# Optimization experiments

Hardware: AMD Instinct MI355X
Metric: run time of the kernel (lower is better)

Reference implementation:

```python
import jax, jax.numpy as jnp
import numpy as np

N = 100000      # nodes
E = 1600000     # edges (avg degree 16)
DIN = 3         # input_dim (xyz coords)
DOUT = 64       # output_dim
EPS = 1e-5      # LayerNorm eps


def setup_inputs() -> dict:
    key = jax.random.key(0)
    ks = jax.random.split(key, 6)
    x = jax.random.normal(ks[0], (N, DIN), jnp.float32)
    edge_index = jax.random.randint(ks[1], (2, E), 0, N, dtype=jnp.int64)
    # li1: Linear(DIN, DOUT)
    W1 = jax.random.normal(ks[2], (DIN, DOUT), jnp.float32) / np.sqrt(DIN)
    b1 = jnp.zeros((DOUT,), jnp.float32)
    # gcn1: GCNConv(DOUT, DOUT) -> weight + bias
    Wg = jax.random.normal(ks[3], (DOUT, DOUT), jnp.float32) / np.sqrt(DOUT)
    bg = jnp.zeros((DOUT,), jnp.float32)
    # norm1d: LayerNorm(2*DOUT)
    gamma = jnp.ones((2 * DOUT,), jnp.float32)
    beta = jnp.zeros((2 * DOUT,), jnp.float32)
    return {"x": x, "edge_index": edge_index, "W1": W1, "b1": b1,
            "Wg": Wg, "bg": bg, "gamma": gamma, "beta": beta}


def reference(x, edge_index, W1, b1, Wg, bg, gamma, beta):
    n = x.shape[0]
    # li1 + act
    h = jax.nn.relu(x @ W1 + b1)                       # [N, DOUT]
    # GCNConv: add self loops, symmetric normalization D^-1/2 (A+I) D^-1/2
    loops = jnp.arange(n, dtype=edge_index.dtype)
    src = jnp.concatenate([edge_index[0], loops])      # [E+N]
    dst = jnp.concatenate([edge_index[1], loops])      # [E+N]
    deg = jax.ops.segment_sum(jnp.ones_like(dst, h.dtype), dst, num_segments=n)
    dinv = jnp.where(deg > 0, jax.lax.rsqrt(jnp.maximum(deg, 1.0)), 0.0)
    norm = dinv[src] * dinv[dst]                       # [E+N]
    hg = h @ Wg                                        # [N, DOUT]
    agg = jax.ops.segment_sum(hg[src] * norm[:, None], dst, num_segments=n)
    h2 = jax.nn.relu(agg + bg)                         # [N, DOUT]
    # concat + LayerNorm(2*DOUT)
    cat = jnp.concatenate([h, h2], axis=1)             # [N, 2*DOUT]
    mu = jnp.mean(cat, axis=-1, keepdims=True)
    var = jnp.mean(jnp.square(cat - mu), axis=-1, keepdims=True)
    return (cat - mu) * jax.lax.rsqrt(var + EPS) * gamma + beta
```

## Files before the change

kernel.cpp:

```cpp
#include <hip/hip_runtime.h>
#include <math.h>

#define N_NODES 100000
#define N_EDGES 1600000
#define EPS_    1e-5f
#define PAD     64
#define SCOL    48


#define NCHUNK_E 782
#define EPB_E    2048
#define NB_EDGE  (NCHUNK_E * 8)
#define PART_SZ  12500

#define LIN_WAVES 1563

typedef float v16f __attribute__((ext_vector_type(16)));

__device__ __forceinline__ float bf2f(unsigned short u) {
    union { unsigned int i; float f; } v; v.i = (unsigned int)u << 16; return v.f;
}
__device__ __forceinline__ unsigned short f2bf(float f) {
    union { float f; unsigned int i; } v; v.f = f;
    unsigned int b = v.i + 0x7FFFu + ((v.i >> 16) & 1u);
    return (unsigned short)(b >> 16);
}
__device__ __forceinline__ unsigned int pk2(float lo, float hi) {
    return (unsigned int)f2bf(lo) | ((unsigned int)f2bf(hi) << 16);
}

#define FMA16(A, wv0, wv1, wv2, wv3)                                          \
    do {                                                                      \
        A[0]  = fmaf(hk, wv0.x, A[0]);  A[1]  = fmaf(hk, wv0.y, A[1]);        \
        A[2]  = fmaf(hk, wv0.z, A[2]);  A[3]  = fmaf(hk, wv0.w, A[3]);        \
        A[4]  = fmaf(hk, wv1.x, A[4]);  A[5]  = fmaf(hk, wv1.y, A[5]);        \
        A[6]  = fmaf(hk, wv1.z, A[6]);  A[7]  = fmaf(hk, wv1.w, A[7]);        \
        A[8]  = fmaf(hk, wv2.x, A[8]);  A[9]  = fmaf(hk, wv2.y, A[9]);        \
        A[10] = fmaf(hk, wv2.z, A[10]); A[11] = fmaf(hk, wv2.w, A[11]);       \
        A[12] = fmaf(hk, wv3.x, A[12]); A[13] = fmaf(hk, wv3.y, A[13]);       \
        A[14] = fmaf(hk, wv3.z, A[14]); A[15] = fmaf(hk, wv3.w, A[15]);       \
    } while (0)

__global__ void fused_edge_lin_kernel(const int* __restrict__ src,
                                      const int* __restrict__ dst,
                                      const float* __restrict__ x,
                                      const float* __restrict__ W1,
                                      const float* __restrict__ b1,
                                      const float* __restrict__ Wg,
                                      int* __restrict__ cnt,
                                      int* __restrict__ ell,
                                      unsigned short* __restrict__ hb_g)
{
    const int tl    = threadIdx.x;
    const int part  = blockIdx.x & 7;
    const int chunk = blockIdx.x >> 3;
    const int lo    = part * PART_SZ;
    const int hi    = lo + PART_SZ;

    const int ebase = chunk * EPB_E + tl * 8;
    int dv[8], sv[8], pos[8];
    if (ebase + 8 <= N_EDGES) {
        const int4 d0 = *(const int4*)(dst + ebase);
        const int4 d1 = *(const int4*)(dst + ebase + 4);
        const int4 s0 = *(const int4*)(src + ebase);
        const int4 s1 = *(const int4*)(src + ebase + 4);
        dv[0] = d0.x; dv[1] = d0.y; dv[2] = d0.z; dv[3] = d0.w;
        dv[4] = d1.x; dv[5] = d1.y; dv[6] = d1.z; dv[7] = d1.w;
        sv[0] = s0.x; sv[1] = s0.y; sv[2] = s0.z; sv[3] = s0.w;
        sv[4] = s1.x; sv[5] = s1.y; sv[6] = s1.z; sv[7] = s1.w;
    } else {
#pragma unroll
        for (int j = 0; j < 8; ++j) {
            const int e = ebase + j;
            if (e < N_EDGES) { dv[j] = dst[e]; sv[j] = src[e]; }
            else             { dv[j] = -1;     sv[j] = 0;      }
        }
    }
#pragma unroll
    for (int j = 0; j < 8; ++j) {
        pos[j] = -1;
        if (dv[j] >= lo && dv[j] < hi) pos[j] = atomicAdd(&cnt[dv[j]], 1);
    }

    const int wave = blockIdx.x * 4 + (tl >> 6);
    if (wave < LIN_WAVES) {
        const int lane = tl & 63;
        const int n    = wave * 64 + lane;
        const bool act = (n < N_NODES);
        float x0 = 0.f, x1 = 0.f, x2 = 0.f;
        if (act) { x0 = x[n * 3]; x1 = x[n * 3 + 1]; x2 = x[n * 3 + 2]; }

        v16f a0, a1, a2, a3;
#pragma unroll
        for (int i = 0; i < 16; ++i) { a0[i] = 0.f; a1[i] = 0.f; a2[i] = 0.f; a3[i] = 0.f; }

        for (int k = 0; k < 64; ++k) {
            const float w0 = W1[k];
            const float w1 = W1[64 + k];
            const float w2 = W1[128 + k];
            const float bb = b1[k];
            const float hk = fmaxf(fmaf(x0, w0, fmaf(x1, w1, fmaf(x2, w2, bb))), 0.f);

            const float4* __restrict__ r4 = (const float4*)(Wg + (size_t)k * 64);
            {
                const float4 p0 = r4[0], p1 = r4[1], p2 = r4[2], p3 = r4[3];
                FMA16(a0, p0, p1, p2, p3);
            }
            {
                const float4 p0 = r4[4], p1 = r4[5], p2 = r4[6], p3 = r4[7];
                FMA16(a1, p0, p1, p2, p3);
            }
            {
                const float4 p0 = r4[8], p1 = r4[9], p2 = r4[10], p3 = r4[11];
                FMA16(a2, p0, p1, p2, p3);
            }
            {
                const float4 p0 = r4[12], p1 = r4[13], p2 = r4[14], p3 = r4[15];
                FMA16(a3, p0, p1, p2, p3);
            }
        }

        if (act) {
            uint4* __restrict__ dp = (uint4*)(hb_g + (size_t)n * 64);
            dp[0] = make_uint4(pk2(a0[0],  a0[1]),  pk2(a0[2],  a0[3]),
                               pk2(a0[4],  a0[5]),  pk2(a0[6],  a0[7]));
            dp[1] = make_uint4(pk2(a0[8],  a0[9]),  pk2(a0[10], a0[11]),
                               pk2(a0[12], a0[13]), pk2(a0[14], a0[15]));
            dp[2] = make_uint4(pk2(a1[0],  a1[1]),  pk2(a1[2],  a1[3]),
                               pk2(a1[4],  a1[5]),  pk2(a1[6],  a1[7]));
            dp[3] = make_uint4(pk2(a1[8],  a1[9]),  pk2(a1[10], a1[11]),
                               pk2(a1[12], a1[13]), pk2(a1[14], a1[15]));
            dp[4] = make_uint4(pk2(a2[0],  a2[1]),  pk2(a2[2],  a2[3]),
                               pk2(a2[4],  a2[5]),  pk2(a2[6],  a2[7]));
            dp[5] = make_uint4(pk2(a2[8],  a2[9]),  pk2(a2[10], a2[11]),
                               pk2(a2[12], a2[13]), pk2(a2[14], a2[15]));
            dp[6] = make_uint4(pk2(a3[0],  a3[1]),  pk2(a3[2],  a3[3]),
                               pk2(a3[4],  a3[5]),  pk2(a3[6],  a3[7]));
            dp[7] = make_uint4(pk2(a3[8],  a3[9]),  pk2(a3[10], a3[11]),
                               pk2(a3[12], a3[13]), pk2(a3[14], a3[15]));
        }
    }

#pragma unroll
    for (int j = 0; j < 8; ++j)
        if (pos[j] >= 0 && pos[j] < PAD) ell[dv[j] * PAD + pos[j]] = sv[j];
}

__global__ void gather_final_kernel(const unsigned short* __restrict__ hb_g,
                                    const int* __restrict__ cnt,
                                    const int* __restrict__ ell,
                                    const float* __restrict__ x,
                                    const float* __restrict__ W1,
                                    const float* __restrict__ b1,
                                    const float* __restrict__ bg,
                                    const float* __restrict__ gamma,
                                    const float* __restrict__ beta,
                                    float* __restrict__ out)
{
    __shared__ int sell[64 * SCOL];
    __shared__ int lcnt[64];
    const int tl = threadIdx.x;
    const int b  = blockIdx.x;
    const int nb = b * 64;

    if (tl < 64) {
        const int n = nb + tl;
        lcnt[tl] = (n < N_NODES) ? cnt[n] : 0;
    }
    {
        const int r = tl >> 2;
        const int q = tl & 3;
        const int nr = nb + r;
        if (nr < N_NODES) {
            const int4* __restrict__ grow = (const int4*)(ell + (size_t)nr * PAD);
            int4* __restrict__ srow = (int4*)(sell + r * SCOL);
            srow[q]     = grow[q];
            srow[q + 4] = grow[q + 4];
            srow[q + 8] = grow[q + 8];
        }
    }
    __syncthreads();

    const int lane = tl & 63;
    const int w    = tl >> 6;
    const float w0 = W1[lane], w1 = W1[64 + lane], w2 = W1[128 + lane];
    const float bb1 = b1[lane];
    const float bgl = bg[lane];
    const float g0 = gamma[lane], g1 = gamma[64 + lane];
    const float be0 = beta[lane], be1 = beta[64 + lane];

    for (int nl = w; nl < 64; nl += 4) {
        const int n = nb + nl;
        if (n >= N_NODES) break;

        const int c    = lcnt[nl];
        const float di = rsqrtf((float)(c + 1));
        const int deg  = (c < PAD) ? c : PAD;
        const int dstg = (deg < SCOL) ? deg : SCOL;
        const int* row = sell + nl * SCOL;

        const float xx0 = x[n * 3], xx1 = x[n * 3 + 1], xx2 = x[n * 3 + 2];
        float acc = di * bf2f(hb_g[(size_t)n * 64 + lane]);

        int j = 0;
        for (; j + 8 <= dstg; j += 8) {
            const int s0 = row[j + 0], s1 = row[j + 1], s2 = row[j + 2], s3 = row[j + 3];
            const int s4 = row[j + 4], s5 = row[j + 5], s6 = row[j + 6], s7 = row[j + 7];
            const float a0 = bf2f(hb_g[(size_t)s0 * 64 + lane]);
            const float a1 = bf2f(hb_g[(size_t)s1 * 64 + lane]);
            const float a2 = bf2f(hb_g[(size_t)s2 * 64 + lane]);
            const float a3 = bf2f(hb_g[(size_t)s3 * 64 + lane]);
            const float a4 = bf2f(hb_g[(size_t)s4 * 64 + lane]);
            const float a5 = bf2f(hb_g[(size_t)s5 * 64 + lane]);
            const float a6 = bf2f(hb_g[(size_t)s6 * 64 + lane]);
            const float a7 = bf2f(hb_g[(size_t)s7 * 64 + lane]);
            const float v0 = rsqrtf((float)(cnt[s0] + 1));
            const float v1 = rsqrtf((float)(cnt[s1] + 1));
            const float v2 = rsqrtf((float)(cnt[s2] + 1));
            const float v3 = rsqrtf((float)(cnt[s3] + 1));
            const float v4 = rsqrtf((float)(cnt[s4] + 1));
            const float v5 = rsqrtf((float)(cnt[s5] + 1));
            const float v6 = rsqrtf((float)(cnt[s6] + 1));
            const float v7 = rsqrtf((float)(cnt[s7] + 1));
            acc = fmaf(v0, a0, acc); acc = fmaf(v1, a1, acc);
            acc = fmaf(v2, a2, acc); acc = fmaf(v3, a3, acc);
            acc = fmaf(v4, a4, acc); acc = fmaf(v5, a5, acc);
            acc = fmaf(v6, a6, acc); acc = fmaf(v7, a7, acc);
        }
        for (; j < dstg; ++j) {
            const int s = row[j];
            acc = fmaf(rsqrtf((float)(cnt[s] + 1)),
                       bf2f(hb_g[(size_t)s * 64 + lane]), acc);
        }
        for (; j < deg; ++j) {
            const int s = ell[(size_t)n * PAD + j];
            acc = fmaf(rsqrtf((float)(cnt[s] + 1)),
                       bf2f(hb_g[(size_t)s * 64 + lane]), acc);
        }

        float h  = fmaxf(fmaf(xx0, w0, fmaf(xx1, w1, fmaf(xx2, w2, bb1))), 0.f);
        float h2 = fmaxf(fmaf(di, acc, bgl), 0.f);

        float sum = h + h2;
#pragma unroll
        for (int o = 32; o > 0; o >>= 1) sum += __shfl_xor(sum, o, 64);
        const float mu = sum * (1.0f / 128.0f);

        const float dA = h  - mu;
        const float dB = h2 - mu;
        float vs = dA * dA + dB * dB;
#pragma unroll
        for (int o = 32; o > 0; o >>= 1) vs += __shfl_xor(vs, o, 64);
        const float rr = rsqrtf(vs * (1.0f / 128.0f) + EPS_);

        out[(size_t)n * 128 + lane]      = dA * rr * g0 + be0;
        out[(size_t)n * 128 + 64 + lane] = dB * rr * g1 + be1;
    }
}

extern "C" void kernel_launch(void* const* d_in, const int* in_sizes, int n_in,
                              void* d_out, int out_size, void* d_ws, size_t ws_size,
                              hipStream_t stream)
{
    const float* x     = (const float*)d_in[0];
    const int*   edge  = (const int*)  d_in[1];
    const float* W1    = (const float*)d_in[2];
    const float* b1    = (const float*)d_in[3];
    const float* Wg    = (const float*)d_in[4];
    const float* bg    = (const float*)d_in[5];
    const float* gamma = (const float*)d_in[6];
    const float* beta  = (const float*)d_in[7];
    float*       out   = (float*)d_out;

    char*  ws  = (char*)d_ws;
    size_t p   = 0;
    unsigned short* hb_g = (unsigned short*)(ws + p); p += (size_t)N_NODES * 64 * sizeof(unsigned short);
    int*            ell  = (int*)           (ws + p); p += (size_t)N_NODES * PAD * sizeof(int);
    int*            cnt  = (int*)           (ws + p);

    const int* src = edge;
    const int* dst = edge + N_EDGES;

    hipMemsetAsync(cnt, 0, (size_t)N_NODES * sizeof(int), stream);

    fused_edge_lin_kernel<<<NB_EDGE, 256, 0, stream>>>(src, dst, x, W1, b1, Wg,
                                                       cnt, ell, hb_g);
    gather_final_kernel<<<(N_NODES + 63) / 64, 256, 0, stream>>>(hb_g, cnt, ell,
                                                                 x, W1, b1,
                                                                 bg, gamma, beta, out);
}
```

Measured before the change: 239.1 us.

## Prescale node features by source degree norm in separate pass before gather

Adds a scale_kernel that multiplies each node's bf16 feature row by rsqrt(deg+1) in place after the edge/linear kernel. The gather kernel then sums neighbor features without loading cnt[s] for every neighbor or computing per-edge rsqrt, and reads the neighbor index lists with int4 vector loads. This removes a random scattered load and a transcendental from each edge. In exchange it adds a kernel launch and a full read-write pass over the 12.8 MB feature buffer, plus an extra bf16 rounding of the scaled values.

Result: faster. 215.2 us (-10.0%).

```diff
diff --git a/kernel.cpp b/kernel.cpp
--- a/kernel.cpp
+++ b/kernel.cpp
@@ -146,6 +146,19 @@
         if (pos[j] >= 0 && pos[j] < PAD) ell[dv[j] * PAD + pos[j]] = sv[j];
 }
 
+__global__ void scale_kernel(const int* __restrict__ cnt,
+                             unsigned int* __restrict__ g2)
+{
+    const int t = blockIdx.x * blockDim.x + threadIdx.x;
+    if (t >= N_NODES * 32) return;
+    const int node = t >> 5;
+    const float di = rsqrtf((float)(cnt[node] + 1));
+    const unsigned int v = g2[t];
+    const float lo = bf2f((unsigned short)(v & 0xFFFFu)) * di;
+    const float hi = bf2f((unsigned short)(v >> 16)) * di;
+    g2[t] = (unsigned int)f2bf(lo) | ((unsigned int)f2bf(hi) << 16);
+}
+
 __global__ void gather_final_kernel(const unsigned short* __restrict__ hb_g,
                                     const int* __restrict__ cnt,
                                     const int* __restrict__ ell,
@@ -200,43 +213,31 @@
         const int* row = sell + nl * SCOL;
 
         const float xx0 = x[n * 3], xx1 = x[n * 3 + 1], xx2 = x[n * 3 + 2];
-        float acc = di * bf2f(hb_g[(size_t)n * 64 + lane]);
+        float acc = bf2f(hb_g[(size_t)n * 64 + lane]);
 
         int j = 0;
         for (; j + 8 <= dstg; j += 8) {
-            const int s0 = row[j + 0], s1 = row[j + 1], s2 = row[j + 2], s3 = row[j + 3];
-            const int s4 = row[j + 4], s5 = row[j + 5], s6 = row[j + 6], s7 = row[j + 7];
-            const float a0 = bf2f(hb_g[(size_t)s0 * 64 + lane]);
-            const float a1 = bf2f(hb_g[(size_t)s1 * 64 + lane]);
-            const float a2 = bf2f(hb_g[(size_t)s2 * 64 + lane]);
-            const float a3 = bf2f(hb_g[(size_t)s3 * 64 + lane]);
-            const float a4 = bf2f(hb_g[(size_t)s4 * 64 + lane]);
-            const float a5 = bf2f(hb_g[(size_t)s5 * 64 + lane]);
-            const float a6 = bf2f(hb_g[(size_t)s6 * 64 + lane]);
-            const float a7 = bf2f(hb_g[(size_t)s7 * 64 + lane]);
-            const float v0 = rsqrtf((float)(cnt[s0] + 1));
-            const float v1 = rsqrtf((float)(cnt[s1] + 1));
-            const float v2 = rsqrtf((float)(cnt[s2] + 1));
-            const float v3 = rsqrtf((float)(cnt[s3] + 1));
-            const float v4 = rsqrtf((float)(cnt[s4] + 1));
-            const float v5 = rsqrtf((float)(cnt[s5] + 1));
-            const float v6 = rsqrtf((float)(cnt[s6] + 1));
-            const float v7 = rsqrtf((float)(cnt[s7] + 1));
-            acc = fmaf(v0, a0, acc); acc = fmaf(v1, a1, acc);
-            acc = fmaf(v2, a2, acc); acc = fmaf(v3, a3, acc);
-            acc = fmaf(v4, a4, acc); acc = fmaf(v5, a5, acc);
-            acc = fmaf(v6, a6, acc); acc = fmaf(v7, a7, acc);
-        }
-        for (; j < dstg; ++j) {
-            const int s = row[j];
-            acc = fmaf(rsqrtf((float)(cnt[s] + 1)),
-                       bf2f(hb_g[(size_t)s * 64 + lane]), acc);
-        }
-        for (; j < deg; ++j) {
-            const int s = ell[(size_t)n * PAD + j];
-            acc = fmaf(rsqrtf((float)(cnt[s] + 1)),
-                       bf2f(hb_g[(size_t)s * 64 + lane]), acc);
-        }
+            const int4 r0 = *(const int4*)(row + j);
+            const int4 r1 = *(const int4*)(row + j + 4);
+            const float a0 = bf2f(hb_g[(size_t)r0.x * 64 + lane]);
+            const float a1 = bf2f(hb_g[(size_t)r0.y * 64 + lane]);
+            const float a2 = bf2f(hb_g[(size_t)r0.z * 64 + lane]);
+            const float a3 = bf2f(hb_g[(size_t)r0.w * 64 + lane]);
+            const float a4 = bf2f(hb_g[(size_t)r1.x * 64 + lane]);
+            const float a5 = bf2f(hb_g[(size_t)r1.y * 64 + lane]);
+            const float a6 = bf2f(hb_g[(size_t)r1.z * 64 + lane]);
+            const float a7 = bf2f(hb_g[(size_t)r1.w * 64 + lane]);
+            acc += ((a0 + a1) + (a2 + a3)) + ((a4 + a5) + (a6 + a7));
+        }
+        if (j + 4 <= dstg) {
+            const int4 r0 = *(const int4*)(row + j);
+            acc += (bf2f(hb_g[(size_t)r0.x * 64 + lane]) + bf2f(hb_g[(size_t)r0.y * 64 + lane]))
+                 + (bf2f(hb_g[(size_t)r0.z * 64 + lane]) + bf2f(hb_g[(size_t)r0.w * 64 + lane]));
+            j += 4;
+        }
+        for (; j < dstg; ++j) acc += bf2f(hb_g[(size_t)row[j] * 64 + lane]);
+        for (; j < deg; ++j)
+            acc += bf2f(hb_g[(size_t)ell[(size_t)n * PAD + j] * 64 + lane]);
 
         float h  = fmaxf(fmaf(xx0, w0, fmaf(xx1, w1, fmaf(xx2, w2, bb1))), 0.f);
         float h2 = fmaxf(fmaf(di, acc, bgl), 0.f);
@@ -285,6 +286,7 @@
 
     fused_edge_lin_kernel<<<NB_EDGE, 256, 0, stream>>>(src, dst, x, W1, b1, Wg,
                                                        cnt, ell, hb_g);
+    scale_kernel<<<(N_NODES * 32 + 255) / 256, 256, 0, stream>>>(cnt, (unsigned int*)hb_g);
     gather_final_kernel<<<(N_NODES + 63) / 64, 256, 0, stream>>>(hb_g, cnt, ell,
                                                                  x, W1, b1,
                                                                  bg, gamma, beta, out);
```
